# Kernel tuning notes

Measured on AMD Instinct MI355X. Metric: run time of the kernel, lower is better.

The kernel has to match this reference:

```python
import jax, jax.numpy as jnp
import numpy as np

EPS = 1e-5


def _vfe(x, w, b, g, beta):
    # x: (B, Nv, Np, Cin) -> (B, Nv, Cout). Linear -> BatchNorm1d(train stats) -> ReLU -> max over points.
    y = jnp.einsum('bnpc,oc->bnpo', x, w) + b
    mu = y.mean(axis=(0, 1, 2))
    var = y.var(axis=(0, 1, 2))  # biased, as used by torch BN normalization
    y = (y - mu) * jax.lax.rsqrt(var + EPS) * g + beta
    y = jax.nn.relu(y)
    return y.max(axis=2)


def _conv_bn_relu(x, w, b, g, beta):
    # x: (B, Cin, D, H, W); w: (Cout, Cin, 3, 3, 3); stride 2, padding 1.
    y = jax.lax.conv_general_dilated(x, w, (2, 2, 2), [(1, 1)] * 3,
                                     dimension_numbers=('NCDHW', 'OIDHW', 'NCDHW'))
    y = y + b[None, :, None, None, None]
    mu = y.mean(axis=(0, 2, 3, 4), keepdims=True)
    var = y.var(axis=(0, 2, 3, 4), keepdims=True)
    y = (y - mu) * jax.lax.rsqrt(var + EPS) * g[None, :, None, None, None] + beta[None, :, None, None, None]
    return jax.nn.relu(y)


def setup_inputs() -> dict:
    key = jax.random.key(0)
    ks = jax.random.split(key, 16)
    B, Nv, Np, Cin = 2, 12000, 32, 5
    VF = 128  # voxel_feat_dim
    OUT = 256  # output_feat_dim
    D, H, W = 20, 128, 128
    s = 0.05
    inp = {
        'voxel_features': jax.random.normal(ks[0], (B, Nv, Np, Cin), jnp.float32),
        'voxel_coords': jax.random.randint(ks[1], (B, Nv, 3), 0, 20, jnp.int32),
        'D': D, 'H': H, 'W': W,
        # VFE1: 5 -> 64
        'w1': jax.random.normal(ks[2], (VF // 2, Cin), jnp.float32) * s,
        'b1': jnp.zeros((VF // 2,), jnp.float32),
        'g1': jnp.ones((VF // 2,), jnp.float32),
        'be1': jnp.zeros((VF // 2,), jnp.float32),
        # VFE2: 64 -> 128
        'w2': jax.random.normal(ks[3], (VF, VF // 2), jnp.float32) * s,
        'b2': jnp.zeros((VF,), jnp.float32),
        'g2': jnp.ones((VF,), jnp.float32),
        'be2': jnp.zeros((VF,), jnp.float32),
        # conv3d_1: 128 -> 128
        'cw1': jax.random.normal(ks[4], (128, VF, 3, 3, 3), jnp.float32) * s,
        'cb1': jnp.zeros((128,), jnp.float32),
        'cg1': jnp.ones((128,), jnp.float32),
        'cbe1': jnp.zeros((128,), jnp.float32),
        # conv3d_2: 128 -> 256
        'cw2': jax.random.normal(ks[5], (256, 128, 3, 3, 3), jnp.float32) * s,
        'cb2': jnp.zeros((256,), jnp.float32),
        'cg2': jnp.ones((256,), jnp.float32),
        'cbe2': jnp.zeros((256,), jnp.float32),
        # conv3d_3: 256 -> 256
        'cw3': jax.random.normal(ks[6], (OUT, 256, 3, 3, 3), jnp.float32) * s,
        'cb3': jnp.zeros((OUT,), jnp.float32),
        'cg3': jnp.ones((OUT,), jnp.float32),
        'cbe3': jnp.zeros((OUT,), jnp.float32),
    }
    return inp


def reference(voxel_features, voxel_coords, D, H, W,
              w1, b1, g1, be1, w2, b2, g2, be2,
              cw1, cb1, cg1, cbe1, cw2, cb2, cg2, cbe2, cw3, cb3, cg3, cbe3):
    # VFE stages
    f = _vfe(voxel_features, w1, b1, g1, be1)   # (B, Nv, 64)
    f = _vfe(f[:, :, None, :] * 1.0 if False else f.reshape(f.shape[0], f.shape[1], 1, -1), w2, b2, g2, be2) if False else None
    # proper: vfe2 operates on (B, Nv, Np, C) but after vfe1 features are (B, Nv, C);
    # torch code passes 3D tensor? No: vfe2 receives (B, Nv, 64) reshaped -- actually torch
    # VFELayer expects 4D; original forward feeds (B, Nv, 64) which unpacks as (B, Nv, 64)->error-free
    # only if treated as (B, Nv, Np=64, C)? We match the documented intent: treat vfe1 output as
    # (B, Nv, 1, 64) so vfe2's max over points is a no-op.
    f1 = _vfe(voxel_features, w1, b1, g1, be1)          # (B, Nv, 64)
    f2 = _vfe(f1[:, :, None, :], w2, b2, g2, be2)       # (B, Nv, 128)
    B, Nv, C = f2.shape
    # scatter voxel features into dense grid (B, C, D, H, W)
    def scat(feat, coords):
        grid = jnp.zeros((C, D, H, W), feat.dtype)
        return grid.at[:, coords[:, 0], coords[:, 1], coords[:, 2]].set(feat.T)
    grid = jax.vmap(scat)(f2, voxel_coords)
    x = _conv_bn_relu(grid, cw1, cb1, cg1, cbe1)
    x = _conv_bn_relu(x, cw2, cb2, cg2, cbe2)
    x = _conv_bn_relu(x, cw3, cb3, cg3, cbe3)
    return x
```

## Files before the change

### kernel.cpp

```cpp
#include <hip/hip_runtime.h>
#include <hip/hip_bf16.h>

#define EPS 1e-5f

#define BB 2
#define NV 12000
#define NP 32
#define CIN 5
#define GD 20

typedef __attribute__((ext_vector_type(8))) short bf16x8;
typedef __attribute__((ext_vector_type(4))) float f32x4;

static const size_t OFF_SX   = 0;
static const size_t OFF_MST  = 32;
static const size_t OFF_AC1  = 4192;
static const size_t OFF_AC2  = 4320;
static const size_t OFF_ACB1 = 4576;
static const size_t OFF_ACB2 = 4960;
static const size_t OFF_AC3  = 7520;
static const size_t OFF_BG2  = 8032;
static const size_t OFF_BG3  = 10080;
static const size_t OFF_W2T  = 13152;
static const size_t OFF_WIN  = 21344;
static const size_t OFF_F1   = 37344;
static const size_t OFF_I0CL = 1573344;
static const size_t OFF_I1   = 3059168;
static const size_t OFF_I2   = 3644896;
static const size_t OFF_WT1B = 4031968;
static const size_t OFF_WT2  = 4253152;
static const size_t OFF_WT3  = 5137888;
static const size_t OFF_RAW1 = 6907360;
static const size_t OFF_RAW2 = 8146400;
static const size_t OFF_RAW3 = 9620960;
static const size_t OFF_MSTP = 10407392;
static const size_t OFF_SXP  = 11472352;


__global__ __launch_bounds__(256) void k_stats_x(const float* __restrict__ vf, float* __restrict__ sxp,
                                                 const int* __restrict__ coords, int* __restrict__ winner) {
    if (blockIdx.x >= 750){
        int i = (blockIdx.x - 750)*256 + threadIdx.x;
        if (i >= BB*NV) return;
        int b = i / NV, n = i % NV;
        int d = coords[(size_t)i*3], h = coords[(size_t)i*3+1], w = coords[(size_t)i*3+2];
        if (d<0||d>=GD||h<0||h>=GD||w<0||w>=GD) return;
        atomicMax(&winner[b*8000 + d*400 + h*20 + w], n);
        return;
    }
    __shared__ float st[5120];
    __shared__ float sw[4*20];
    int t = threadIdx.x;
    const float4* src = (const float4*)(vf + (size_t)blockIdx.x*5120);
    #pragma unroll
    for (int i=0;i<5;i++) ((float4*)st)[i*256 + t] = src[i*256 + t];
    __syncthreads();
    float vals[20];
    #pragma unroll
    for (int i=0;i<20;i++) vals[i]=0.f;
    const float* base = st + t*20;
    #pragma unroll
    for (int p=0;p<4;p++){
        const float* v = base + p*5;
        int k=5;
        #pragma unroll
        for (int c=0;c<5;c++){
            vals[c]+=v[c];
            #pragma unroll
            for(int c2=c;c2<5;c2++){ vals[k++]+=v[c]*v[c2]; }
        }
    }
    #pragma unroll
    for (int off=32; off>0; off>>=1){
        #pragma unroll
        for (int i=0;i<20;i++) vals[i] += __shfl_down(vals[i], off);
    }
    int wave = t>>6, lane = t&63;
    if (lane==0){
        #pragma unroll
        for (int i=0;i<20;i++) sw[wave*20+i]=vals[i];
    }
    __syncthreads();
    if (t<20){
        float s = sw[t]+sw[20+t]+sw[40+t]+sw[60+t];
        sxp[(size_t)t*768 + blockIdx.x] = s;
    }
}

__global__ __launch_bounds__(256) void k_red_sx_ac1(const float* __restrict__ sxp,
                                                    const float* __restrict__ w1, const float* __restrict__ b1,
                                                    const float* __restrict__ g1, const float* __restrict__ be1,
                                                    float* __restrict__ AC1){
    __shared__ float S[20];
    int t = threadIdx.x;
    int wave = t>>6, lane = t&63;
    for (int c = wave; c < 20; c += 4){
        float s = 0.f;
        for (int b = lane; b < 750; b += 64) s += sxp[(size_t)c*768 + b];
        #pragma unroll
        for (int off=32; off>0; off>>=1) s += __shfl_down(s, off);
        if (lane==0) S[c] = s;
    }
    __syncthreads();
    int o = t; if (o>=64) return;
    const float N = (float)(BB*NV*NP);
    float w[5];
    #pragma unroll
    for(int c=0;c<5;c++) w[c]=w1[o*5+c];
    float b=b1[o];
    float wd=0;
    #pragma unroll
    for(int c=0;c<5;c++) wd += w[c]*S[c];
    float m = wd/N + b;
    float q=0; int kk=5;
    for(int c=0;c<5;c++) for(int c2=c;c2<5;c2++){ float s=S[kk++]; q += (c==c2?1.f:2.f)*w[c]*w[c2]*s; }
    q = q/N + 2.f*b*wd/N + b*b;
    float var = q - m*m;
    float A = g1[o]*rsqrtf(var + EPS);
    AC1[o] = A;
    AC1[64+o] = be1[o] + (b - m)*A;
}

__global__ __launch_bounds__(256) void k_vfe1(const float* __restrict__ vf, const float* __restrict__ w1,
                                              const float* __restrict__ AC1, float* __restrict__ f1){
    int wave = threadIdx.x >> 6;
    int lane = threadIdx.x & 63;
    int v = blockIdx.x*4 + wave;
    if (v >= BB*NV) return;
    float w[5];
    #pragma unroll
    for (int c=0;c<5;c++) w[c] = w1[lane*5+c];
    float A = AC1[lane], Cc = AC1[64+lane];
    const float* x = vf + (size_t)v*(NP*CIN);
    float mx = -1e30f;
    #pragma unroll
    for (int pc = 0; pc < 8; pc++) {
        float xx[20];
        const float4* x4 = (const float4*)(x + pc*20);
        #pragma unroll
        for (int i=0;i<5;i++){ float4 t = x4[i]; xx[4*i]=t.x; xx[4*i+1]=t.y; xx[4*i+2]=t.z; xx[4*i+3]=t.w; }
        #pragma unroll
        for (int j=0;j<4;j++){
            float y = xx[j*5]*w[0]+xx[j*5+1]*w[1]+xx[j*5+2]*w[2]+xx[j*5+3]*w[3]+xx[j*5+4]*w[4];
            mx = fmaxf(mx, y*A + Cc);
        }
    }
    f1[(size_t)v*64 + lane] = fmaxf(mx, 0.f);
}

__global__ __launch_bounds__(256) void k_stats_f1(const float* __restrict__ f1, float* __restrict__ Mpart){
    __shared__ float tile[16][64];
    __shared__ float ssum[64];
    int t = threadIdx.x;
    if (t < 64) ssum[t]=0.f;
    float acc[4][4];
    #pragma unroll
    for(int i=0;i<4;i++)
        #pragma unroll
        for(int j=0;j<4;j++) acc[i][j]=0.f;
    int i4 = (t>>4)*4, j4 = (t&15)*4;
    const int NT = (BB*NV)/16;
    for (int tl = blockIdx.x; tl < NT; tl += gridDim.x) {
        __syncthreads();
        for (int i = t; i < 16*64; i += 256) tile[i>>6][i&63] = f1[(size_t)tl*1024 + i];
        __syncthreads();
        #pragma unroll
        for (int r=0;r<16;r++){
            float a[4], bb[4];
            #pragma unroll
            for (int u=0;u<4;u++) a[u]=tile[r][i4+u];
            #pragma unroll
            for (int u=0;u<4;u++) bb[u]=tile[r][j4+u];
            #pragma unroll
            for (int u=0;u<4;u++)
                #pragma unroll
                for (int q=0;q<4;q++) acc[u][q] += a[u]*bb[q];
        }
        if (t < 64) {
            float s=0;
            #pragma unroll
            for(int r=0;r<16;r++) s+=tile[r][t];
            ssum[t]+=s;
        }
    }
    float* mp = Mpart + (size_t)blockIdx.x*4160;
    #pragma unroll
    for(int i=0;i<4;i++)
        #pragma unroll
        for(int j=0;j<4;j++) mp[(size_t)(i4+i)*64 + (j4+j)] = acc[i][j];
    __syncthreads();
    if (t<64) mp[4096 + t] = ssum[t];
}

__global__ __launch_bounds__(64) void k_red_mst(const float* __restrict__ Mpart, float* __restrict__ Mst){
    int e = blockIdx.x*64 + threadIdx.x;
    if (e >= 4160) return;
    float s = 0.f;
    #pragma unroll 8
    for (int p=0;p<256;p++) s += Mpart[(size_t)p*4160 + e];
    Mst[e] = s;
}

__global__ __launch_bounds__(64) void k_ac2(const float* __restrict__ Mst, const float* __restrict__ w2,
                                            const float* __restrict__ b2, const float* __restrict__ g2,
                                            const float* __restrict__ be2, float* __restrict__ AC2){
    int o = blockIdx.x;
    int j = threadIdx.x;
    const float N = (float)(BB*NV);
    const float* M = Mst; const float* sv = Mst+4096;
    const float* wrow = w2 + o*64;
    float wj = wrow[j];
    float sj = 0.f;
    #pragma unroll 8
    for (int c=0;c<64;c++) sj += wrow[c]*M[c*64+j];
    float q = wj*sj;
    float wdp = wj*sv[j];
    #pragma unroll
    for (int off=32; off>0; off>>=1){ q += __shfl_down(q,off); wdp += __shfl_down(wdp,off); }
    if (j==0){
        float b = b2[o];
        float m = wdp/N + b;
        float qq = q/N + 2.f*b*wdp/N + b*b;
        float var = qq - m*m;
        float A = g2[o]*rsqrtf(var+EPS);
        AC2[o]=A; AC2[128+o]= be2[o] + (b-m)*A;
    }
}


__global__ __launch_bounds__(256) void k_I0(const int* __restrict__ winner, const float* __restrict__ f1,
                                            const float* __restrict__ w2T, const float* __restrict__ AC2,
                                            __hip_bfloat16* __restrict__ I0cl){
    int blk = blockIdx.x;
    int b = blk / 400; int dh = blk % 400;
    int d = dh / 20, h = dh % 20;
    __shared__ int win[20];
    __shared__ float f1sh[20][64];
    __shared__ float sh[20*128];
    int t = threadIdx.x;
    if (t < 20) win[t] = winner[b*8000 + dh*20 + t];
    __syncthreads();
    for (int idx = t; idx < 1280; idx += 256){
        int cell = idx >> 6, c = idx & 63;
        int n = win[cell];
        f1sh[cell][c] = (n>=0) ? f1[((size_t)(b*NV+n))*64 + c] : 0.f;
    }
    __syncthreads();
    int o = t & 127;
    int half = t >> 7;
    float A = AC2[o], C = AC2[128+o];
    for (int p=0;p<10;p++){
        int cell = p*2 + half;
        float acc = 0.f;
        if (win[cell] >= 0){
            #pragma unroll
            for (int c=0;c<64;c++) acc += f1sh[cell][c]*w2T[c*128+o];
            acc = fmaxf(acc*A + C, 0.f);
        }
        sh[cell*128 + o] = acc;
    }
    __syncthreads();
    __hip_bfloat16* outp = I0cl + (((size_t)(b*21 + d+1)*23 + h+1)*24 + 1)*128;
    for (int idx = t; idx < 2560; idx += 256) outp[idx] = __float2bfloat16(sh[idx]);
}

__global__ __launch_bounds__(256) void k_t_tile(const float* __restrict__ cw2, const float* __restrict__ cw3,
                                                const float* __restrict__ w2, const float* __restrict__ cw1,
                                                float* __restrict__ wT2, float* __restrict__ wT3,
                                                float* __restrict__ w2T, __hip_bfloat16* __restrict__ wT1b,
                                                float* __restrict__ I0z, float* __restrict__ bgz,
                                                int* __restrict__ winp){
    int blk = blockIdx.x;
    int t = threadIdx.x;
    if (blk >= 1141){
        int4* d = (int4*)winp;
        int4 mone; mone.x=-1; mone.y=-1; mone.z=-1; mone.w=-1;
        #pragma unroll
        for (int k=0;k<16;k++){
            int idx = k*256 + t;
            if (idx < 4000) d[idx] = mone;
        }
        return;
    }
    if (blk == 1140){
        float4 z; z.x=0.f; z.y=0.f; z.z=0.f; z.w=0.f;
        float4* d = (float4*)bgz;
        #pragma unroll
        for (int k=0;k<5;k++) d[k*256 + t] = z;
        return;
    }
    if (blk >= 777){
        float4 z; z.x=0.f; z.y=0.f; z.z=0.f; z.w=0.f;
        float4* d = (float4*)I0z;
        int base = (blk - 777)*1024;
        #pragma unroll
        for (int k=0;k<4;k++){
            int idx = base + k*256 + t;
            if (idx < 371456) d[idx] = z;
        }
        return;
    }
    if (blk >= 649){
        int co = blk - 649;
        __shared__ float tlw[3456];
        for (int j=t; j<3456; j+=256) tlw[j] = cw1[(size_t)co*3456 + j];
        __syncthreads();
        for (int idx=t; idx<3456; idx+=256){
            int tap = idx >> 7, ci = idx & 127;
            wT1b[((size_t)(tap*128 + co) << 7) + ci] = __float2bfloat16(tlw[ci*27 + tap]);
        }
        return;
    }
    if (blk == 648){
        for (int i=t; i<8192; i+=256){ int o=i>>6, c=i&63; w2T[c*128+o]=w2[i]; }
        return;
    }
    const float* src; float* dst; int CO, R;
    if (blk < 216){ src=cw2; dst=wT2; CO=256; R=3456; }
    else { blk-=216; src=cw3; dst=wT3; CO=256; R=6912; }
    int nrt = R/64;
    int rt = blk % nrt, ct = blk / nrt;
    int r0 = rt*64, c0 = ct*64;
    __shared__ float tl[64][65];
    int tj = threadIdx.x & 63;
    int ti0 = threadIdx.x >> 6;
    #pragma unroll
    for (int k=0;k<16;k++){
        int i = ti0 + k*4;
        tl[i][tj] = src[(size_t)(c0+i)*R + r0 + tj];
    }
    __syncthreads();
    #pragma unroll
    for (int k=0;k<16;k++){
        int j = ti0 + k*4;
        dst[(size_t)(r0+j)*CO + c0 + tj] = tl[tj][j];
    }
}

__global__ __launch_bounds__(256) void k_conv1m(const __hip_bfloat16* __restrict__ I0cl,
                                                const __hip_bfloat16* __restrict__ wT1b,
                                                float* __restrict__ raw1){
    int blk = blockIdx.x;
    int oh = blk % 11; int r2 = blk / 11;
    int od = r2 % 10; int b = r2 / 10;
    __shared__ float4 ldsv[3456];
    char* lds = (char*)ldsv;
    int t = threadIdx.x;
    for (int i = t; i < 3456; i += 256){
        int row = i >> 4;
        int dh = row / 24, w = row % 24;
        int dd = dh / 3, hh = dh % 3;
        const char* src = (const char*)(I0cl + (((size_t)(b*21 + 2*od+dd)*23 + 2*oh+hh)*24 + w)*128);
        float4 v = *(const float4*)(src + (i & 15)*16);
        int lb = i*16;
        *(float4*)(lds + (lb ^ ((row & 7) << 4))) = v;
    }
    __syncthreads();
    int wave = t >> 6, lane = t & 63;
    int col = lane & 15, quad = lane >> 4;
    int co0 = wave*32;
    f32x4 acc0 = {0.f,0.f,0.f,0.f};
    f32x4 acc1 = {0.f,0.f,0.f,0.f};
    for (int kd=0; kd<3; kd++){
        for (int kh=0; kh<3; kh++){
            #pragma unroll
            for (int kw=0; kw<3; kw++){
                int tap = (kd*3+kh)*3 + kw;
                int wi = 2*col + kw; if (wi > 23) wi = 23;
                int row = (kd*3+kh)*24 + wi;
                int lbbase = (row << 8) + quad*16;
                int xr = (row & 7) << 4;
                const __hip_bfloat16* ap0 = wT1b + (size_t)tap*16384 + (co0 + col)*128 + quad*8;
                #pragma unroll
                for (int q=0; q<4; q++){
                    bf16x8 b0 = *(const bf16x8*)(lds + ((lbbase + q*64) ^ xr));
                    bf16x8 a0 = *(const bf16x8*)(ap0 + q*32);
                    bf16x8 a1 = *(const bf16x8*)(ap0 + q*32 + 2048);
                    acc0 = __builtin_amdgcn_mfma_f32_16x16x32_bf16(a0, b0, acc0, 0, 0, 0);
                    acc1 = __builtin_amdgcn_mfma_f32_16x16x32_bf16(a1, b0, acc1, 0, 0, 0);
                }
            }
        }
    }
    if (col < 11){
        #pragma unroll
        for (int r=0;r<4;r++){
            int co = co0 + quad*4 + r;
            raw1[(((size_t)(b*128+co)*10 + od)*11 + oh)*11 + col] = acc0[r];
        }
        #pragma unroll
        for (int r=0;r<4;r++){
            int co = co0 + 16 + quad*4 + r;
            raw1[(((size_t)(b*128+co)*10 + od)*11 + oh)*11 + col] = acc1[r];
        }
    }
}

__global__ __launch_bounds__(256) void k_stats_c1(const float* __restrict__ raw1, const float* __restrict__ cb,
                                                  const float* __restrict__ cg, const float* __restrict__ cbe,
                                                  float* __restrict__ ACb1){
    int co = blockIdx.x;
    float s=0, ss=0;
    for (int b=0;b<2;b++){
        size_t base = ((size_t)(b*128+co))*1210;
        for (int i=threadIdx.x; i<1210; i+=256){
            float v = raw1[base+i];
            s+=v; ss+=v*v;
        }
    }
    __shared__ float sh1[256], sh2[256];
    sh1[threadIdx.x]=s; sh2[threadIdx.x]=ss; __syncthreads();
    for (int st=128; st>0; st>>=1){
        if (threadIdx.x<st){ sh1[threadIdx.x]+=sh1[threadIdx.x+st]; sh2[threadIdx.x]+=sh2[threadIdx.x+st]; }
        __syncthreads();
    }
    if (threadIdx.x==0){
        float bias = cb[co];
        const float N = 81920.f;
        float sum_y = sh1[0] + N*bias;
        float ssq_y = sh2[0] + 2.f*bias*sh1[0] + N*bias*bias;
        float m = sum_y/N;
        float var = ssq_y/N - m*m;
        float A = cg[co]*rsqrtf(var+EPS);
        float C = cbe[co] - m*A;
        ACb1[co]=A; ACb1[128+co]=C;
        ACb1[256+co]=fmaxf(bias*A + C, 0.f);
    }
}

__global__ __launch_bounds__(256) void k_fill_I1_bg2(const float* __restrict__ raw1, const float* __restrict__ ACb1,
                                                     const float* __restrict__ cb, float* __restrict__ I1p,
                                                     const float* __restrict__ cw2, float* __restrict__ bgraw2){
    if (blockIdx.x >= 2288){
        int o = blockIdx.x - 2288;
        int t = threadIdx.x;
        float acc[8];
        #pragma unroll
        for (int c=0;c<8;c++) acc[c]=0.f;
        if (t < 128){
            int ci = t;
            float w[27];
            const float* wp = cw2 + (size_t)o*3456 + ci*27;
            #pragma unroll
            for (int k=0;k<27;k++) w[k] = wp[k];
            float bg = ACb1[256+ci];
            float sw0[9], sw1[9];
            #pragma unroll
            for (int t9=0;t9<9;t9++){ sw1[t9]=w[3*t9+1]+w[3*t9+2]; sw0[t9]=w[3*t9]+sw1[t9]; }
            #pragma unroll
            for (int cls=0; cls<8; cls++){
                const int d0=(cls>>2)&1, h0=(cls>>1)&1, w0=cls&1;
                float ws=0.f;
                #pragma unroll
                for (int kd=0;kd<3;kd++){
                    if (d0 && kd==0) continue;
                    #pragma unroll
                    for (int kh=0;kh<3;kh++){
                        if (h0 && kh==0) continue;
                        ws += w0 ? sw1[kd*3+kh] : sw0[kd*3+kh];
                    }
                }
                acc[cls] = bg*ws;
            }
        }
        #pragma unroll
        for (int off=32; off>0; off>>=1){
            #pragma unroll
            for (int c=0;c<8;c++) acc[c] += __shfl_down(acc[c], off);
        }
        __shared__ float sred[4][8];
        if ((t&63)==0){
            #pragma unroll
            for (int c=0;c<8;c++) sred[t>>6][c] = acc[c];
        }
        __syncthreads();
        if (t < 8) bgraw2[o*8+t] = sred[0][t]+sred[1][t]+sred[2][t]+sred[3][t];
        return;
    }
    int i = blockIdx.x*blockDim.x + threadIdx.x;
    int wpad = i % 16; int r = i / 16;
    int hpad = r % 13; r /= 13;
    int dpad = r % 11; r /= 11;
    int ci = r % 128; int b = r / 128;
    float val;
    if (dpad==0 || hpad==0 || wpad==0 || wpad>12) val = 0.f;
    else {
        int d = dpad-1, h = hpad-1, w = wpad-1;
        if (h < 11 && w < 11){
            size_t idx = (((size_t)(b*128+ci)*10 + d)*11 + h)*11 + w;
            val = fmaxf((raw1[idx] + cb[ci])*ACb1[ci] + ACb1[128+ci], 0.f);
        } else val = ACb1[256+ci];
    }
    I1p[i] = val;
}

__global__ __launch_bounds__(256) void k_conv2(const float* __restrict__ I1p, const float* __restrict__ wT2,
                                               float* __restrict__ raw2){
    int blk = blockIdx.x;
    int ciq = blk & 15; blk >>= 4;
    int oh = blk % 6; blk /= 6;
    int od = blk % 5; int b = blk / 5;
    int wave = threadIdx.x >> 6, lane = threadIdx.x & 63;
    float acc[4][6];
    #pragma unroll
    for (int q=0;q<4;q++)
        #pragma unroll
        for (int i=0;i<6;i++) acc[q][i]=0.f;
    int ci0 = ciq*8 + wave*2;
    for (int ci = ci0; ci < ci0+2; ci++){
        const float* base = I1p + ((size_t)(b*128+ci)*11 + 2*od)*208 + (2*oh)*16;
        const float* wp0 = wT2 + (size_t)ci*27*256 + lane;
        #pragma unroll
        for (int kd=0;kd<3;kd++){
            #pragma unroll
            for (int kh=0;kh<3;kh++){
                float row[16];
                const float4* rp = (const float4*)(base + kd*208 + kh*16);
                #pragma unroll
                for (int i=0;i<4;i++){ float4 t=rp[i]; row[4*i]=t.x; row[4*i+1]=t.y; row[4*i+2]=t.z; row[4*i+3]=t.w; }
                const float* wp = wp0 + (kd*3+kh)*3*256;
                #pragma unroll
                for (int kw=0;kw<3;kw++){
                    float w0=wp[kw*256], w1=wp[kw*256+64], w2v=wp[kw*256+128], w3=wp[kw*256+192];
                    #pragma unroll
                    for (int ow=0;ow<6;ow++){
                        float x = row[2*ow+kw];
                        acc[0][ow]+=x*w0; acc[1][ow]+=x*w1; acc[2][ow]+=x*w2v; acc[3][ow]+=x*w3;
                    }
                }
            }
        }
    }
    __shared__ float red[4*1540];
    #pragma unroll
    for (int q=0;q<4;q++)
        #pragma unroll
        for (int ow=0;ow<6;ow++) red[wave*1540 + lane*24 + q*6 + ow] = acc[q][ow];
    __syncthreads();
    float* rb = raw2 + (size_t)ciq*92160;
    for (int idx = threadIdx.x; idx < 1536; idx += 256){
        int lane2 = idx/24, j = idx%24;
        float s = red[0*1540 + lane2*24 + j] + red[1*1540 + lane2*24 + j]
                + red[2*1540 + lane2*24 + j] + red[3*1540 + lane2*24 + j];
        int q = j/6, ow = j%6;
        int co = q*64 + lane2;
        rb[(((size_t)(b*256+co)*5 + od)*6 + oh)*6 + ow] = s;
    }
}

__global__ __launch_bounds__(64) void k_stats_c2(const float* __restrict__ raw2, const float* __restrict__ bgraw2,
                                                 const float* __restrict__ cb2, const float* __restrict__ cg2,
                                                 const float* __restrict__ cbe2, float* __restrict__ ACb2){
    int o = blockIdx.x;
    int lane = threadIdx.x;
    float s=0.f, ss=0.f;
    for (int idx=lane; idx<360; idx+=64){
        int b = idx/180; int p = idx%180;
        int d = p/36; int rem = p%36; int h = rem/6; int w = rem%6;
        size_t base = (((size_t)(b*256+o)*5 + d)*6 + h)*6 + w;
        float v = 0.f;
        #pragma unroll
        for (int q=0;q<16;q++) v += raw2[q*92160+base];
        s += v; ss += v*v;
    }
    #pragma unroll
    for (int off=32; off>0; off>>=1){ s += __shfl_down(s,off); ss += __shfl_down(ss,off); }
    if (lane==0){
        const int n2[8] = {3744,104,104,0,936,26,26,0};
        float bgv[8];
        #pragma unroll
        for (int c=0;c<8;c++){ bgv[c]=bgraw2[o*8+c]; s += 2.f*n2[c]*bgv[c]; ss += 2.f*n2[c]*bgv[c]*bgv[c]; }
        const float N = 10240.f;
        float b = cb2[o];
        float sum_y = s + N*b;
        float ssq_y = ss + 2.f*b*s + N*b*b;
        float m = sum_y/N;
        float var = ssq_y/N - m*m;
        float A = cg2[o]*rsqrtf(var+EPS); float C = cbe2[o] - m*A;
        ACb2[o]=A; ACb2[256+o]=C;
        for (int c=0;c<8;c++) ACb2[512+o*8+c] = fmaxf((bgv[c]+b)*A + C, 0.f);
    }
}

__global__ __launch_bounds__(256) void k_fill_I2_bg3(const float* __restrict__ raw2, const float* __restrict__ ACb2,
                                                     const float* __restrict__ cb2, float* __restrict__ I2p,
                                                     const float* __restrict__ cw3, float* __restrict__ bgraw3){
    if (blockIdx.x >= 1512){
        int o = blockIdx.x - 1512;
        int t = threadIdx.x;
        float sum12[12];
        {
            int ci = t;
            float w[27];
            const float* wp = cw3 + ((size_t)o*256 + ci)*27;
            #pragma unroll
            for (int k=0;k<27;k++) w[k] = wp[k];
            const float* bg = ACb2 + 512 + ci*8;
            float bgv[8];
            #pragma unroll
            for (int q=0;q<8;q++) bgv[q]=bg[q];
            #pragma unroll
            for (int c=0;c<12;c++){
                const int odc = c>>2; const int h0 = (c>>1)&1; const int w0 = c&1;
                float sum = 0.f;
                #pragma unroll
                for (int kd=0;kd<3;kd++){
                    const int d = 2*odc-1+kd; if (d<0||d>=5) continue;
                    const int db = (d==0)?4:0;
                    #pragma unroll
                    for (int kh=0;kh<3;kh++){
                        if (h0 && kh==0) continue;
                        const int hb = (h0 && kh==1)?2:0;
                        #pragma unroll
                        for (int kw=0;kw<3;kw++){
                            if (w0 && kw==0) continue;
                            const int wb = (w0 && kw==1)?1:0;
                            sum += bgv[db|hb|wb]*w[(kd*3+kh)*3+kw];
                        }
                    }
                }
                sum12[c] = sum;
            }
        }
        #pragma unroll
        for (int off=32; off>0; off>>=1){
            #pragma unroll
            for (int c=0;c<12;c++) sum12[c] += __shfl_down(sum12[c], off);
        }
        __shared__ float sred[4][12];
        if ((t&63)==0){
            #pragma unroll
            for (int c=0;c<12;c++) sred[t>>6][c] = sum12[c];
        }
        __syncthreads();
        if (t < 12) bgraw3[o*12+t] = sred[0][t]+sred[1][t]+sred[2][t]+sred[3][t];
        return;
    }
    int i = blockIdx.x*blockDim.x + threadIdx.x;
    int wpad = i % 12; int r = i / 12;
    int hpad = r % 9; r /= 9;
    int dpad = r % 7; r /= 7;
    int ci = r % 256; int b = r / 256;
    float val;
    if (dpad==0 || dpad==6 || hpad==0 || wpad==0 || wpad>8) val = 0.f;
    else {
        int d = dpad-1, h = hpad-1, w = wpad-1;
        if (h<6 && w<6){
            size_t idx = (((size_t)(b*256+ci)*5 + d)*6 + h)*6 + w;
            float raw = 0.f;
            #pragma unroll
            for (int q=0;q<16;q++) raw += raw2[q*92160+idx];
            val = fmaxf((raw + cb2[ci])*ACb2[ci] + ACb2[256+ci], 0.f);
        } else {
            int cls = ((d==0)?4:0) | ((h==0)?2:0) | ((w==0)?1:0);
            val = ACb2[512 + ci*8 + cls];
        }
    }
    I2p[i] = val;
}

__global__ __launch_bounds__(256) void k_conv3(const float* __restrict__ I2p, const float* __restrict__ wT3,
                                               float* __restrict__ raw3){
    int blk = blockIdx.x;
    int ciq = blk & 31; blk >>= 5;
    int oh = blk % 4; blk /= 4;
    int od = blk % 3; int b = blk / 3;
    int wave = threadIdx.x >> 6, lane = threadIdx.x & 63;
    float acc[4][4];
    #pragma unroll
    for (int q=0;q<4;q++)
        #pragma unroll
        for (int i=0;i<4;i++) acc[q][i]=0.f;
    int ci0 = ciq*8 + wave*2;
    for (int ci = ci0; ci < ci0+2; ci++){
        const float* base = I2p + ((size_t)(b*256+ci)*7 + 2*od)*108 + (2*oh)*12;
        const float* wp0 = wT3 + (size_t)ci*27*256 + lane;
        #pragma unroll
        for (int kd=0;kd<3;kd++){
            #pragma unroll
            for (int kh=0;kh<3;kh++){
                float row[12];
                const float4* rp = (const float4*)(base + kd*108 + kh*12);
                #pragma unroll
                for (int i=0;i<3;i++){ float4 t=rp[i]; row[4*i]=t.x; row[4*i+1]=t.y; row[4*i+2]=t.z; row[4*i+3]=t.w; }
                const float* wp = wp0 + (kd*3+kh)*3*256;
                #pragma unroll
                for (int kw=0;kw<3;kw++){
                    float w0=wp[kw*256], w1=wp[kw*256+64], w2v=wp[kw*256+128], w3=wp[kw*256+192];
                    #pragma unroll
                    for (int ow=0;ow<4;ow++){
                        float x = row[2*ow+kw];
                        acc[0][ow]+=x*w0; acc[1][ow]+=x*w1; acc[2][ow]+=x*w2v; acc[3][ow]+=x*w3;
                    }
                }
            }
        }
    }
    __shared__ float red[4*1028];
    #pragma unroll
    for (int q=0;q<4;q++)
        #pragma unroll
        for (int ow=0;ow<4;ow++) red[wave*1028 + lane*16 + q*4 + ow] = acc[q][ow];
    __syncthreads();
    float* rb = raw3 + (size_t)ciq*24576;
    for (int idx = threadIdx.x; idx < 1024; idx += 256){
        int lane2 = idx/16, j = idx%16;
        float s = red[0*1028 + lane2*16 + j] + red[1*1028 + lane2*16 + j]
                + red[2*1028 + lane2*16 + j] + red[3*1028 + lane2*16 + j];
        int q = j/4, ow = j%4;
        int co = q*64 + lane2;
        rb[(((size_t)(b*256+co)*3 + od)*4 + oh)*4 + ow] = s;
    }
}

__global__ __launch_bounds__(64) void k_stats_c3(const float* __restrict__ raw3, const float* __restrict__ bgraw3,
                                                 const float* __restrict__ cb3, const float* __restrict__ cg3,
                                                 const float* __restrict__ cbe3, float* __restrict__ AC3){
    int o = blockIdx.x;
    int lane = threadIdx.x;
    float s=0.f, ss=0.f;
    for (int idx=lane; idx<96; idx+=64){
        int b = idx/48; int p = idx%48;
        int d = p/16; int rem = p%16; int h = rem/4; int w = rem%4;
        size_t base = (((size_t)(b*256+o)*3 + d)*4 + h)*4 + w;
        float v = 0.f;
        #pragma unroll
        for (int q=0;q<32;q++) v += raw3[q*24576+base];
        s += v; ss += v*v;
    }
    #pragma unroll
    for (int off=32; off>0; off>>=1){ s += __shfl_down(s,off); ss += __shfl_down(ss,off); }
    if (lane==0){
        const int n3hw[4] = {216,12,12,0};
        for (int c=0;c<12;c++){
            float bg = bgraw3[o*12+c];
            float n = 2.f*n3hw[c&3];
            s += n*bg; ss += n*bg*bg;
        }
        const float N = 1536.f;
        float b = cb3[o];
        float sum_y = s + N*b;
        float ssq_y = ss + 2.f*b*s + N*b*b;
        float m = sum_y/N;
        float var = ssq_y/N - m*m;
        float A = cg3[o]*rsqrtf(var+EPS);
        AC3[o]=A; AC3[256+o]=cbe3[o] - m*A;
    }
}

__global__ void k_final(const float* __restrict__ raw3, const float* __restrict__ bgraw3,
                        const float* __restrict__ cb3, const float* __restrict__ AC3,
                        float* __restrict__ out){
    int i = blockIdx.x*blockDim.x + threadIdx.x;
    if (i >= 2*256*3*16*16) return;
    int ow = i % 16; int r = i / 16;
    int oh = r % 16; r /= 16;
    int od = r % 3; r /= 3;
    int o = r % 256; int b = r / 256;
    float v;
    if (oh<4 && ow<4){
        size_t base = (((size_t)(b*256+o)*3 + od)*4 + oh)*4 + ow;
        v = 0.f;
        #pragma unroll
        for (int q=0;q<32;q++) v += raw3[q*24576+base];
    } else {
        v = bgraw3[o*12 + od*4 + ((oh==0)?2:0) + ((ow==0)?1:0)];
    }
    out[i] = fmaxf((v + cb3[o])*AC3[o] + AC3[256+o], 0.f);
}


extern "C" void kernel_launch(void* const* d_in, const int* in_sizes, int n_in,
                              void* d_out, int out_size, void* d_ws, size_t ws_size,
                              hipStream_t stream) {
    const float* vf    = (const float*)d_in[0];
    const int*   coords= (const int*)d_in[1];
    const float* w1    = (const float*)d_in[5];
    const float* b1    = (const float*)d_in[6];
    const float* g1    = (const float*)d_in[7];
    const float* be1   = (const float*)d_in[8];
    const float* w2    = (const float*)d_in[9];
    const float* b2    = (const float*)d_in[10];
    const float* g2    = (const float*)d_in[11];
    const float* be2   = (const float*)d_in[12];
    const float* cw1   = (const float*)d_in[13];
    const float* cb1   = (const float*)d_in[14];
    const float* cg1   = (const float*)d_in[15];
    const float* cbe1  = (const float*)d_in[16];
    const float* cw2   = (const float*)d_in[17];
    const float* cb2   = (const float*)d_in[18];
    const float* cg2   = (const float*)d_in[19];
    const float* cbe2  = (const float*)d_in[20];
    const float* cw3   = (const float*)d_in[21];
    const float* cb3   = (const float*)d_in[22];
    const float* cg3   = (const float*)d_in[23];
    const float* cbe3  = (const float*)d_in[24];
    float* out = (float*)d_out;
    float* ws  = (float*)d_ws;
    __hip_bfloat16* I0cl = (__hip_bfloat16*)(ws + OFF_I0CL);
    __hip_bfloat16* wT1b = (__hip_bfloat16*)(ws + OFF_WT1B);
    int* winp = (int*)(ws + OFF_WIN);

    k_t_tile<<<1142,256,0,stream>>>(cw2, cw3, w2, cw1, ws+OFF_WT2, ws+OFF_WT3, ws+OFF_W2T, wT1b,
                                    ws+OFF_I0CL, ws+OFF_BG2, winp);
    k_stats_x<<<844,256,0,stream>>>(vf, ws+OFF_SXP, coords, winp);
    k_red_sx_ac1<<<1,256,0,stream>>>(ws+OFF_SXP, w1,b1,g1,be1, ws+OFF_AC1);
    k_vfe1<<<6000,256,0,stream>>>(vf, w1, ws+OFF_AC1, ws+OFF_F1);
    k_stats_f1<<<256,256,0,stream>>>(ws+OFF_F1, ws+OFF_MSTP);
    k_red_mst<<<65,64,0,stream>>>(ws+OFF_MSTP, ws+OFF_MST);
    k_ac2<<<128,64,0,stream>>>(ws+OFF_MST, w2,b2,g2,be2, ws+OFF_AC2);
    k_I0<<<800,256,0,stream>>>(winp, ws+OFF_F1, ws+OFF_W2T, ws+OFF_AC2, I0cl);
    k_conv1m<<<220,256,0,stream>>>(I0cl, wT1b, ws+OFF_RAW1);
    k_stats_c1<<<128,256,0,stream>>>(ws+OFF_RAW1, cb1,cg1,cbe1, ws+OFF_ACB1);
    k_fill_I1_bg2<<<2544,256,0,stream>>>(ws+OFF_RAW1, ws+OFF_ACB1, cb1, ws+OFF_I1, cw2, ws+OFF_BG2);
    k_conv2<<<960,256,0,stream>>>(ws+OFF_I1, ws+OFF_WT2, ws+OFF_RAW2);
    k_stats_c2<<<256,64,0,stream>>>(ws+OFF_RAW2, ws+OFF_BG2, cb2, cg2, cbe2, ws+OFF_ACB2);
    k_fill_I2_bg3<<<1768,256,0,stream>>>(ws+OFF_RAW2, ws+OFF_ACB2, cb2, ws+OFF_I2, cw3, ws+OFF_BG3);
    k_conv3<<<768,256,0,stream>>>(ws+OFF_I2, ws+OFF_WT3, ws+OFF_RAW3);
    k_stats_c3<<<256,64,0,stream>>>(ws+OFF_RAW3, ws+OFF_BG3, cb3, cg3, cbe3, ws+OFF_AC3);
    k_final<<<1536,256,0,stream>>>(ws+OFF_RAW3, ws+OFF_BG3, cb3, ws+OFF_AC3, out);
}
```

Measured before the change: 321.6 us.

## Fuse front-end kernels and defer VFE1 affine via per-voxel max/min

Merges the weight transposes, zero fills, input statistics and the VFE1 linear pass into one kernel. VFE1 now stores the per-voxel max and min of the raw linear output, so the BN affine and ReLU can be applied later: the max is used when the scale is non-negative and the min otherwise. This lets VFE1 run without waiting for the batch statistics. The winner atomics move into the stats reduction kernel, and k_I0 now keeps w2T weights in registers. The cost is an extra intermediate buffer pair (aliased onto RAW2) and extra reads in the f1 statistics kernel.

```diff
diff --git a/kernel.cpp b/kernel.cpp
--- a/kernel.cpp
+++ b/kernel.cpp
@@ -36,11 +36,153 @@
 static const size_t OFF_MSTP = 10407392;
 static const size_t OFF_SXP  = 11472352;
 
-
-__global__ __launch_bounds__(256) void k_stats_x(const float* __restrict__ vf, float* __restrict__ sxp,
-                                                 const int* __restrict__ coords, int* __restrict__ winner) {
-    if (blockIdx.x >= 750){
-        int i = (blockIdx.x - 750)*256 + threadIdx.x;
+__global__ __launch_bounds__(256) void k_front(const float* __restrict__ cw2, const float* __restrict__ cw3,
+                                               const float* __restrict__ w2, const float* __restrict__ cw1,
+                                               float* __restrict__ wT2, float* __restrict__ wT3,
+                                               float* __restrict__ w2T, __hip_bfloat16* __restrict__ wT1b,
+                                               float* __restrict__ I0z, float* __restrict__ bgz,
+                                               int* __restrict__ winp,
+                                               const float* __restrict__ vf, float* __restrict__ sxp,
+                                               const float* __restrict__ w1,
+                                               float* __restrict__ mxb, float* __restrict__ mnb){
+    __shared__ float shm[5200];
+    int blk = blockIdx.x;
+    int t = threadIdx.x;
+    if (blk >= 1892){
+        int wave = t >> 6, lane = t & 63;
+        int v = (blk - 1892)*4 + wave;
+        float w[5];
+        #pragma unroll
+        for (int c=0;c<5;c++) w[c] = w1[lane*5+c];
+        const float* x = vf + (size_t)v*(NP*CIN);
+        float mx = -1e30f, mn = 1e30f;
+        #pragma unroll
+        for (int pc = 0; pc < 8; pc++) {
+            float xx[20];
+            const float4* x4 = (const float4*)(x + pc*20);
+            #pragma unroll
+            for (int i=0;i<5;i++){ float4 q = x4[i]; xx[4*i]=q.x; xx[4*i+1]=q.y; xx[4*i+2]=q.z; xx[4*i+3]=q.w; }
+            #pragma unroll
+            for (int j=0;j<4;j++){
+                float y = xx[j*5]*w[0]+xx[j*5+1]*w[1]+xx[j*5+2]*w[2]+xx[j*5+3]*w[3]+xx[j*5+4]*w[4];
+                mx = fmaxf(mx, y); mn = fminf(mn, y);
+            }
+        }
+        mxb[(size_t)v*64 + lane] = mx;
+        mnb[(size_t)v*64 + lane] = mn;
+        return;
+    }
+    if (blk >= 1142){
+        int sb = blk - 1142;
+        float* st = shm; float* sw = shm + 5120;
+        const float4* src = (const float4*)(vf + (size_t)sb*5120);
+        #pragma unroll
+        for (int i=0;i<5;i++) ((float4*)st)[i*256 + t] = src[i*256 + t];
+        __syncthreads();
+        float vals[20];
+        #pragma unroll
+        for (int i=0;i<20;i++) vals[i]=0.f;
+        const float* base = st + t*20;
+        #pragma unroll
+        for (int p=0;p<4;p++){
+            const float* v2 = base + p*5;
+            int k=5;
+            #pragma unroll
+            for (int c=0;c<5;c++){
+                vals[c]+=v2[c];
+                #pragma unroll
+                for(int c2=c;c2<5;c2++){ vals[k++]+=v2[c]*v2[c2]; }
+            }
+        }
+        #pragma unroll
+        for (int off=32; off>0; off>>=1){
+            #pragma unroll
+            for (int i=0;i<20;i++) vals[i] += __shfl_down(vals[i], off);
+        }
+        int wave = t>>6, lane = t&63;
+        if (lane==0){
+            #pragma unroll
+            for (int i=0;i<20;i++) sw[wave*20+i]=vals[i];
+        }
+        __syncthreads();
+        if (t<20){
+            float s = sw[t]+sw[20+t]+sw[40+t]+sw[60+t];
+            sxp[(size_t)t*768 + sb] = s;
+        }
+        return;
+    }
+    if (blk >= 1141){
+        int4* d = (int4*)winp;
+        int4 mone; mone.x=-1; mone.y=-1; mone.z=-1; mone.w=-1;
+        #pragma unroll
+        for (int k=0;k<16;k++){
+            int idx = k*256 + t;
+            if (idx < 4000) d[idx] = mone;
+        }
+        return;
+    }
+    if (blk == 1140){
+        float4 z; z.x=0.f; z.y=0.f; z.z=0.f; z.w=0.f;
+        float4* d = (float4*)bgz;
+        #pragma unroll
+        for (int k=0;k<5;k++) d[k*256 + t] = z;
+        return;
+    }
+    if (blk >= 777){
+        float4 z; z.x=0.f; z.y=0.f; z.z=0.f; z.w=0.f;
+        float4* d = (float4*)I0z;
+        int base = (blk - 777)*1024;
+        #pragma unroll
+        for (int k=0;k<4;k++){
+            int idx = base + k*256 + t;
+            if (idx < 371456) d[idx] = z;
+        }
+        return;
+    }
+    if (blk >= 649){
+        int co = blk - 649;
+        float* tlw = shm;
+        for (int j=t; j<3456; j+=256) tlw[j] = cw1[(size_t)co*3456 + j];
+        __syncthreads();
+        for (int idx=t; idx<3456; idx+=256){
+            int tap = idx >> 7, ci = idx & 127;
+            wT1b[((size_t)(tap*128 + co) << 7) + ci] = __float2bfloat16(tlw[ci*27 + tap]);
+        }
+        return;
+    }
+    if (blk == 648){
+        for (int i=t; i<8192; i+=256){ int o=i>>6, c=i&63; w2T[c*128+o]=w2[i]; }
+        return;
+    }
+    const float* src; float* dst; int CO, R;
+    if (blk < 216){ src=cw2; dst=wT2; CO=256; R=3456; }
+    else { blk-=216; src=cw3; dst=wT3; CO=256; R=6912; }
+    int nrt = R/64;
+    int rt = blk % nrt, ct = blk / nrt;
+    int r0 = rt*64, c0 = ct*64;
+    float (*tl)[65] = (float(*)[65])shm;
+    int tj = threadIdx.x & 63;
+    int ti0 = threadIdx.x >> 6;
+    #pragma unroll
+    for (int k=0;k<16;k++){
+        int i = ti0 + k*4;
+        tl[i][tj] = src[(size_t)(c0+i)*R + r0 + tj];
+    }
+    __syncthreads();
+    #pragma unroll
+    for (int k=0;k<16;k++){
+        int j = ti0 + k*4;
+        dst[(size_t)(r0+j)*CO + c0 + tj] = tl[tj][j];
+    }
+}
+
+__global__ __launch_bounds__(256) void k_red_sx_ac1(const float* __restrict__ sxp,
+                                                    const float* __restrict__ w1, const float* __restrict__ b1,
+                                                    const float* __restrict__ g1, const float* __restrict__ be1,
+                                                    float* __restrict__ AC1,
+                                                    const int* __restrict__ coords, int* __restrict__ winner){
+    if (blockIdx.x >= 1){
+        int i = (blockIdx.x - 1)*256 + threadIdx.x;
         if (i >= BB*NV) return;
         int b = i / NV, n = i % NV;
         int d = coords[(size_t)i*3], h = coords[(size_t)i*3+1], w = coords[(size_t)i*3+2];
@@ -48,49 +190,6 @@
         atomicMax(&winner[b*8000 + d*400 + h*20 + w], n);
         return;
     }
-    __shared__ float st[5120];
-    __shared__ float sw[4*20];
-    int t = threadIdx.x;
-    const float4* src = (const float4*)(vf + (size_t)blockIdx.x*5120);
-    #pragma unroll
-    for (int i=0;i<5;i++) ((float4*)st)[i*256 + t] = src[i*256 + t];
-    __syncthreads();
-    float vals[20];
-    #pragma unroll
-    for (int i=0;i<20;i++) vals[i]=0.f;
-    const float* base = st + t*20;
-    #pragma unroll
-    for (int p=0;p<4;p++){
-        const float* v = base + p*5;
-        int k=5;
-        #pragma unroll
-        for (int c=0;c<5;c++){
-            vals[c]+=v[c];
-            #pragma unroll
-            for(int c2=c;c2<5;c2++){ vals[k++]+=v[c]*v[c2]; }
-        }
-    }
-    #pragma unroll
-    for (int off=32; off>0; off>>=1){
-        #pragma unroll
-        for (int i=0;i<20;i++) vals[i] += __shfl_down(vals[i], off);
-    }
-    int wave = t>>6, lane = t&63;
-    if (lane==0){
-        #pragma unroll
-        for (int i=0;i<20;i++) sw[wave*20+i]=vals[i];
-    }
-    __syncthreads();
-    if (t<20){
-        float s = sw[t]+sw[20+t]+sw[40+t]+sw[60+t];
-        sxp[(size_t)t*768 + blockIdx.x] = s;
-    }
-}
-
-__global__ __launch_bounds__(256) void k_red_sx_ac1(const float* __restrict__ sxp,
-                                                    const float* __restrict__ w1, const float* __restrict__ b1,
-                                                    const float* __restrict__ g1, const float* __restrict__ be1,
-                                                    float* __restrict__ AC1){
     __shared__ float S[20];
     int t = threadIdx.x;
     int wave = t>>6, lane = t&63;
@@ -121,38 +220,14 @@
     AC1[64+o] = be1[o] + (b - m)*A;
 }
 
-__global__ __launch_bounds__(256) void k_vfe1(const float* __restrict__ vf, const float* __restrict__ w1,
-                                              const float* __restrict__ AC1, float* __restrict__ f1){
-    int wave = threadIdx.x >> 6;
-    int lane = threadIdx.x & 63;
-    int v = blockIdx.x*4 + wave;
-    if (v >= BB*NV) return;
-    float w[5];
-    #pragma unroll
-    for (int c=0;c<5;c++) w[c] = w1[lane*5+c];
-    float A = AC1[lane], Cc = AC1[64+lane];
-    const float* x = vf + (size_t)v*(NP*CIN);
-    float mx = -1e30f;
-    #pragma unroll
-    for (int pc = 0; pc < 8; pc++) {
-        float xx[20];
-        const float4* x4 = (const float4*)(x + pc*20);
-        #pragma unroll
-        for (int i=0;i<5;i++){ float4 t = x4[i]; xx[4*i]=t.x; xx[4*i+1]=t.y; xx[4*i+2]=t.z; xx[4*i+3]=t.w; }
-        #pragma unroll
-        for (int j=0;j<4;j++){
-            float y = xx[j*5]*w[0]+xx[j*5+1]*w[1]+xx[j*5+2]*w[2]+xx[j*5+3]*w[3]+xx[j*5+4]*w[4];
-            mx = fmaxf(mx, y*A + Cc);
-        }
-    }
-    f1[(size_t)v*64 + lane] = fmaxf(mx, 0.f);
-}
-
-__global__ __launch_bounds__(256) void k_stats_f1(const float* __restrict__ f1, float* __restrict__ Mpart){
+__global__ __launch_bounds__(256) void k_stats_f1p(const float* __restrict__ mxb, const float* __restrict__ mnb,
+                                                   const float* __restrict__ AC1,
+                                                   float* __restrict__ f1, float* __restrict__ Mpart){
+    __shared__ float Ash[64], Csh[64];
     __shared__ float tile[16][64];
     __shared__ float ssum[64];
     int t = threadIdx.x;
-    if (t < 64) ssum[t]=0.f;
+    if (t < 64){ Ash[t]=AC1[t]; Csh[t]=AC1[64+t]; ssum[t]=0.f; }
     float acc[4][4];
     #pragma unroll
     for(int i=0;i<4;i++)
@@ -162,7 +237,15 @@
     const int NT = (BB*NV)/16;
     for (int tl = blockIdx.x; tl < NT; tl += gridDim.x) {
         __syncthreads();
-        for (int i = t; i < 16*64; i += 256) tile[i>>6][i&63] = f1[(size_t)tl*1024 + i];
+        for (int i = t; i < 16*64; i += 256){
+            int o = i & 63;
+            float a = Ash[o];
+            float vmx = mxb[(size_t)tl*1024 + i];
+            float vmn = mnb[(size_t)tl*1024 + i];
+            float f = fmaxf(a*((a>=0.f)?vmx:vmn) + Csh[o], 0.f);
+            tile[i>>6][o] = f;
+            f1[(size_t)tl*1024 + i] = f;
+        }
         __syncthreads();
         #pragma unroll
         for (int r=0;r<16;r++){
@@ -249,12 +332,15 @@
     int o = t & 127;
     int half = t >> 7;
     float A = AC2[o], C = AC2[128+o];
+    float wreg[64];
+    #pragma unroll
+    for (int c=0;c<64;c++) wreg[c] = w2T[c*128+o];
     for (int p=0;p<10;p++){
         int cell = p*2 + half;
         float acc = 0.f;
         if (win[cell] >= 0){
             #pragma unroll
-            for (int c=0;c<64;c++) acc += f1sh[cell][c]*w2T[c*128+o];
+            for (int c=0;c<64;c++) acc += f1sh[cell][c]*wreg[c];
             acc = fmaxf(acc*A + C, 0.f);
         }
         sh[cell*128 + o] = acc;
@@ -262,79 +348,6 @@
     __syncthreads();
     __hip_bfloat16* outp = I0cl + (((size_t)(b*21 + d+1)*23 + h+1)*24 + 1)*128;
     for (int idx = t; idx < 2560; idx += 256) outp[idx] = __float2bfloat16(sh[idx]);
-}
-
-__global__ __launch_bounds__(256) void k_t_tile(const float* __restrict__ cw2, const float* __restrict__ cw3,
-                                                const float* __restrict__ w2, const float* __restrict__ cw1,
-                                                float* __restrict__ wT2, float* __restrict__ wT3,
-                                                float* __restrict__ w2T, __hip_bfloat16* __restrict__ wT1b,
-                                                float* __restrict__ I0z, float* __restrict__ bgz,
-                                                int* __restrict__ winp){
-    int blk = blockIdx.x;
-    int t = threadIdx.x;
-    if (blk >= 1141){
-        int4* d = (int4*)winp;
-        int4 mone; mone.x=-1; mone.y=-1; mone.z=-1; mone.w=-1;
-        #pragma unroll
-        for (int k=0;k<16;k++){
-            int idx = k*256 + t;
-            if (idx < 4000) d[idx] = mone;
-        }
-        return;
-    }
-    if (blk == 1140){
-        float4 z; z.x=0.f; z.y=0.f; z.z=0.f; z.w=0.f;
-        float4* d = (float4*)bgz;
-        #pragma unroll
-        for (int k=0;k<5;k++) d[k*256 + t] = z;
-        return;
-    }
-    if (blk >= 777){
-        float4 z; z.x=0.f; z.y=0.f; z.z=0.f; z.w=0.f;
-        float4* d = (float4*)I0z;
-        int base = (blk - 777)*1024;
-        #pragma unroll
-        for (int k=0;k<4;k++){
-            int idx = base + k*256 + t;
-            if (idx < 371456) d[idx] = z;
-        }
-        return;
-    }
-    if (blk >= 649){
-        int co = blk - 649;
-        __shared__ float tlw[3456];
-        for (int j=t; j<3456; j+=256) tlw[j] = cw1[(size_t)co*3456 + j];
-        __syncthreads();
-        for (int idx=t; idx<3456; idx+=256){
-            int tap = idx >> 7, ci = idx & 127;
-            wT1b[((size_t)(tap*128 + co) << 7) + ci] = __float2bfloat16(tlw[ci*27 + tap]);
-        }
-        return;
-    }
-    if (blk == 648){
-        for (int i=t; i<8192; i+=256){ int o=i>>6, c=i&63; w2T[c*128+o]=w2[i]; }
-        return;
-    }
-    const float* src; float* dst; int CO, R;
-    if (blk < 216){ src=cw2; dst=wT2; CO=256; R=3456; }
-    else { blk-=216; src=cw3; dst=wT3; CO=256; R=6912; }
-    int nrt = R/64;
-    int rt = blk % nrt, ct = blk / nrt;
-    int r0 = rt*64, c0 = ct*64;
-    __shared__ float tl[64][65];
-    int tj = threadIdx.x & 63;
-    int ti0 = threadIdx.x >> 6;
-    #pragma unroll
-    for (int k=0;k<16;k++){
-        int i = ti0 + k*4;
-        tl[i][tj] = src[(size_t)(c0+i)*R + r0 + tj];
-    }
-    __syncthreads();
-    #pragma unroll
-    for (int k=0;k<16;k++){
-        int j = ti0 + k*4;
-        dst[(size_t)(r0+j)*CO + c0 + tj] = tl[tj][j];
-    }
 }
 
 __global__ __launch_bounds__(256) void k_conv1m(const __hip_bfloat16* __restrict__ I0cl,
@@ -800,13 +813,13 @@
     __hip_bfloat16* I0cl = (__hip_bfloat16*)(ws + OFF_I0CL);
     __hip_bfloat16* wT1b = (__hip_bfloat16*)(ws + OFF_WT1B);
     int* winp = (int*)(ws + OFF_WIN);
-
-    k_t_tile<<<1142,256,0,stream>>>(cw2, cw3, w2, cw1, ws+OFF_WT2, ws+OFF_WT3, ws+OFF_W2T, wT1b,
-                                    ws+OFF_I0CL, ws+OFF_BG2, winp);
-    k_stats_x<<<844,256,0,stream>>>(vf, ws+OFF_SXP, coords, winp);
-    k_red_sx_ac1<<<1,256,0,stream>>>(ws+OFF_SXP, w1,b1,g1,be1, ws+OFF_AC1);
-    k_vfe1<<<6000,256,0,stream>>>(vf, w1, ws+OFF_AC1, ws+OFF_F1);
-    k_stats_f1<<<256,256,0,stream>>>(ws+OFF_F1, ws+OFF_MSTP);
+    float* mxb = ws + OFF_RAW2;
+    float* mnb = ws + OFF_RAW2 + 768000;
+
+    k_front<<<7892,256,0,stream>>>(cw2, cw3, w2, cw1, ws+OFF_WT2, ws+OFF_WT3, ws+OFF_W2T, wT1b,
+                                   ws+OFF_I0CL, ws+OFF_BG2, winp, vf, ws+OFF_SXP, w1, mxb, mnb);
+    k_red_sx_ac1<<<95,256,0,stream>>>(ws+OFF_SXP, w1,b1,g1,be1, ws+OFF_AC1, coords, winp);
+    k_stats_f1p<<<256,256,0,stream>>>(mxb, mnb, ws+OFF_AC1, ws+OFF_F1, ws+OFF_MSTP);
     k_red_mst<<<65,64,0,stream>>>(ws+OFF_MSTP, ws+OFF_MST);
     k_ac2<<<128,64,0,stream>>>(ws+OFF_MST, w2,b2,g2,be2, ws+OFF_AC2);
     k_I0<<<800,256,0,stream>>>(winp, ws+OFF_F1, ws+OFF_W2T, ws+OFF_AC2, I0cl);
```

Measured after the change: 303.5 us. 5.6% less time.
